# Optimization experiments

Measured on AMD Instinct MI355X. Metric: run time of the kernel, lower is better.

The kernel has to match this reference:

```python
import jax, jax.numpy as jnp
import numpy as np

N, F_IN, HID, H1, NG = 50000, 128, 64, 4, 512
E = 800000


def setup_inputs() -> dict:
    key = jax.random.key(0)
    ks = jax.random.split(key, 16)
    x = jax.random.normal(ks[0], (N, F_IN), dtype=jnp.float32)
    edge_index = jax.random.randint(ks[1], (2, E), 0, N, dtype=jnp.int64)
    batch = jnp.sort(jax.random.randint(ks[2], (N,), 0, NG, dtype=jnp.int64))
    s = 0.05
    W1 = jax.random.normal(ks[3], (F_IN, H1 * HID), dtype=jnp.float32) * s
    a_src1 = jax.random.normal(ks[4], (H1, HID), dtype=jnp.float32) * s
    a_dst1 = jax.random.normal(ks[5], (H1, HID), dtype=jnp.float32) * s
    b1 = jnp.zeros((H1 * HID,), dtype=jnp.float32)
    W2 = jax.random.normal(ks[6], (H1 * HID, HID), dtype=jnp.float32) * s
    a_src2 = jax.random.normal(ks[7], (1, HID), dtype=jnp.float32) * s
    a_dst2 = jax.random.normal(ks[8], (1, HID), dtype=jnp.float32) * s
    b2 = jnp.zeros((HID,), dtype=jnp.float32)
    Wc = jax.random.normal(ks[9], (HID, 2), dtype=jnp.float32) * s
    bc = jnp.zeros((2,), dtype=jnp.float32)
    return dict(x=x, edge_index=edge_index, batch=batch, W1=W1, a_src1=a_src1,
                a_dst1=a_dst1, b1=b1, W2=W2, a_src2=a_src2, a_dst2=a_dst2,
                b2=b2, Wc=Wc, bc=bc)


def gat_layer(x, W, a_src, a_dst, bias, src, dst, n):
    # PyG GATConv: h = x @ W per head; e_ij = LeakyReLU(a_src.h_j + a_dst.h_i),
    # softmax over incoming edges of each dst node, then scatter-add aggregate.
    H, D = a_src.shape
    h = (x @ W).reshape(n, H, D)                       # [N,H,D]
    asrc = jnp.einsum('nhd,hd->nh', h, a_src)          # [N,H]
    adst = jnp.einsum('nhd,hd->nh', h, a_dst)
    e = jax.nn.leaky_relu(asrc[src] + adst[dst], 0.2)  # [E,H]
    m = jax.lax.stop_gradient(jax.ops.segment_max(e, dst, num_segments=n))
    p = jnp.exp(e - m[dst])
    s = jax.ops.segment_sum(p, dst, num_segments=n)
    alpha = p / (s[dst] + 1e-16)                       # [E,H]
    out = jax.ops.segment_sum(alpha[:, :, None] * h[src], dst, num_segments=n)
    return out.reshape(n, H * D) + bias


def reference(x, edge_index, batch, W1, a_src1, a_dst1, b1, W2, a_src2, a_dst2, b2, Wc, bc):
    n = x.shape[0]
    loops = jnp.arange(n, dtype=edge_index.dtype)
    src = jnp.concatenate([edge_index[0], loops])  # add self-loops (PyG default)
    dst = jnp.concatenate([edge_index[1], loops])
    h = jax.nn.relu(gat_layer(x, W1, a_src1, a_dst1, b1, src, dst, n))
    h = jax.nn.relu(gat_layer(h, W2, a_src2, a_dst2, b2, src, dst, n))
    # global mean pool over graphs
    ng = NG
    sums = jax.ops.segment_sum(h, batch, num_segments=ng)
    cnts = jax.ops.segment_sum(jnp.ones((n,), h.dtype), batch, num_segments=ng)
    pooled = sums / jnp.maximum(cnts, 1.0)[:, None]
    logits = pooled @ Wc + bc
    return jax.nn.log_softmax(logits, axis=1)
```

## Files before the change

kernel.cpp:

```cpp
#include <hip/hip_runtime.h>
#include <hip/hip_bf16.h>
#include <cstddef>
#include <cstdint>

#define FIN   128
#define HID   64
#define H1    4
#define NGRAPH 512
#define BCAP  8192

typedef short bf16x8 __attribute__((ext_vector_type(8)));
typedef float f32x4  __attribute__((ext_vector_type(4)));

#if defined(__has_builtin)
#if __has_builtin(__builtin_amdgcn_cvt_f32_fp8) && __has_builtin(__builtin_amdgcn_cvt_pk_fp8_f32)
#define HAVE_HW_FP8 1
#endif
#endif

__device__ __forceinline__ float wave_reduce_sum(float v) {
  #pragma unroll
  for (int off = 32; off > 0; off >>= 1) v += __shfl_down(v, off, 64);
  return v;
}

__device__ __forceinline__ float leaky02(float x) {
  return x > 0.0f ? x : 0.2f * x;
}

__device__ __forceinline__ unsigned short f2bf(float f) {
  union { float f; unsigned int i; } v; v.f = f;
  unsigned int b = v.i;
  return (unsigned short)((b + 0x7FFFu + ((b >> 16) & 1u)) >> 16);
}

#ifndef HAVE_HW_FP8
__device__ __forceinline__ unsigned char f2fp8_1(float f) {
  unsigned int u = __float_as_uint(f);
  unsigned int s = u >> 31;
  u &= 0x7fffffffu;
  if (u > 0x43e00000u) u = 0x43e00000u;
  unsigned int b = u + (0x0007FFFFu + ((u >> 20) & 1u));
  int e = (int)(b >> 23) - 127;
  unsigned int m = (b >> 20) & 7u;
  unsigned char o;
  if (e < -9) o = 0;
  else if (e < -6) { int sh = -6 - e; o = (unsigned char)((8u | m) >> sh); }
  else if (e > 8) o = 0x7e;
  else o = (unsigned char)(((e + 7) << 3) | m);
  return o | (unsigned char)(s << 7);
}
__device__ __forceinline__ float fp8tof_1(unsigned char b) {
  unsigned int s = b >> 7, e = (b >> 3) & 15u, m = b & 7u;
  float v = (e == 0) ? (float)m * 0.001953125f
                     : (float)(8u + m) * __uint_as_float((117u + e) << 23);
  return s ? -v : v;
}
#endif

__device__ __forceinline__ unsigned char f2fp8(float f) {
#ifdef HAVE_HW_FP8
  return (unsigned char)(__builtin_amdgcn_cvt_pk_fp8_f32(f, f, 0u, false) & 0xffu);
#else
  return f2fp8_1(f);
#endif
}
__device__ __forceinline__ float fp8dec(unsigned int w, int i) {
#ifdef HAVE_HW_FP8
  switch (i) {
    case 0: return __builtin_amdgcn_cvt_f32_fp8(w, 0);
    case 1: return __builtin_amdgcn_cvt_f32_fp8(w, 1);
    case 2: return __builtin_amdgcn_cvt_f32_fp8(w, 2);
    default: return __builtin_amdgcn_cvt_f32_fp8(w, 3);
  }
#else
  return fp8tof_1((unsigned char)((w >> (8 * i)) & 0xffu));
#endif
}

#define P3K 16
__global__ __launch_bounds__(256)
void bpart_kernel(const int* __restrict__ src, const int* __restrict__ dst,
                  int* __restrict__ bucketFill, unsigned int* __restrict__ bucketBuf,
                  const float* __restrict__ W1, const float* __restrict__ W2,
                  unsigned short* __restrict__ W1T, unsigned short* __restrict__ W2T,
                  const int* __restrict__ batch, int* __restrict__ gstart,
                  int* __restrict__ gend, int E, int N, int nbuck) {
  int tid = threadIdx.x;
  int stride = gridDim.x * 256;
  int t0 = blockIdx.x * 256 + tid;
  for (int u = t0; u < 256 * 128; u += stride) {
    int n = u >> 7, k = u & 127;
    W1T[u] = f2bf(W1[(size_t)k * 256 + n]);
  }
  for (int u = t0; u < 64 * 256; u += stride) {
    int n = u >> 8, k = u & 255;
    W2T[u] = f2bf(W2[(size_t)k * 64 + n]);
  }
  for (int i = t0; i < N; i += stride) {
    int g = batch[i];
    if (i == 0 || batch[i - 1] != g) gstart[g] = i;
    if (i == N - 1 || batch[i + 1] != g) gend[g] = i + 1;
  }

  __shared__ int lhist[256];
  __shared__ int lbase[256];
  int chunk = 256 * P3K;
  for (int start = blockIdx.x * chunk; start < E; start += gridDim.x * chunk) {
    lhist[tid] = 0;
    __syncthreads();
    int mybuck[P3K]; unsigned int mypack[P3K]; int myrank[P3K];
    #pragma unroll
    for (int k = 0; k < P3K; k++) {
      int i = start + k * 256 + tid;
      if (i < E) {
        int d = dst[i];
        int b = d >> 8;
        mybuck[k] = b;
        mypack[k] = (unsigned int)src[i] | ((unsigned int)(d & 255) << 16);
        myrank[k] = atomicAdd(&lhist[b], 1);
      } else mybuck[k] = -1;
    }
    __syncthreads();
    if (tid < nbuck) lbase[tid] = (lhist[tid] > 0) ? atomicAdd(&bucketFill[tid], lhist[tid]) : 0;
    __syncthreads();
    #pragma unroll
    for (int k = 0; k < P3K; k++) {
      if (mybuck[k] >= 0) {
        int b = mybuck[k];
        int pos = lbase[b] + myrank[k];
        if (pos < BCAP) bucketBuf[((size_t)b << 13) + pos] = mypack[k];
      }
    }
    __syncthreads();
  }
}

__global__ __launch_bounds__(256)
void bbuild_kernel(const unsigned int* __restrict__ bucketBuf, const int* __restrict__ bucketFill,
                   int* __restrict__ rowstart, int* __restrict__ rowend,
                   unsigned short* __restrict__ csr, int N) {
  __shared__ int ldeg[256];
  __shared__ int lscan[256];
  __shared__ int lfill[256];
  int b = blockIdx.x;
  int tid = threadIdx.x;
  int r0 = b << 13;
  int cnt = bucketFill[b]; if (cnt > BCAP) cnt = BCAP;
  int nb0 = b << 8;
  ldeg[tid] = 0;
  __syncthreads();
  for (int j = tid; j < cnt; j += 256)
    atomicAdd(&ldeg[bucketBuf[r0 + j] >> 16], 1);
  __syncthreads();
  int v = ldeg[tid];
  lscan[tid] = v;
  __syncthreads();
  for (int off = 1; off < 256; off <<= 1) {
    int u = (tid >= off) ? lscan[tid - off] : 0;
    __syncthreads();
    lscan[tid] += u;
    __syncthreads();
  }
  int excl = lscan[tid] - v;
  lfill[tid] = excl;
  if (nb0 + tid < N) {
    rowstart[nb0 + tid] = r0 + excl;
    rowend[nb0 + tid]   = r0 + excl + v;
  }
  __syncthreads();
  for (int j = tid; j < cnt; j += 256) {
    unsigned int p = bucketBuf[r0 + j];
    int pos = r0 + atomicAdd(&lfill[p >> 16], 1);
    csr[pos] = (unsigned short)(p & 0xffffu);
  }
}

__global__ __launch_bounds__(256)
void gemm1_kernel(const float* __restrict__ X, const unsigned short* __restrict__ W1T,
                  unsigned char* __restrict__ h1f8,
                  const float* __restrict__ a_src, const float* __restrict__ a_dst,
                  float* __restrict__ asv, float* __restrict__ adv, int N) {
  __shared__ unsigned short As[64][136];
  __shared__ unsigned short Bs[256][40];
  int t = threadIdx.x;
  int w = t >> 6, lane = t & 63;
  int quad = lane >> 4, l16 = lane & 15;
  int blockRow = blockIdx.x * 64;

  {
    int node = t >> 2, kp = (t & 3) * 32;
    int gn = blockRow + node; if (gn >= N) gn = N - 1;
    const float4* xp = (const float4*)(X + (size_t)gn * 128 + kp);
    #pragma unroll
    for (int i = 0; i < 4; i++) {
      float4 va = xp[2 * i], vb = xp[2 * i + 1];
      union { unsigned short u[8]; uint4 v; } r;
      r.u[0] = f2bf(va.x); r.u[1] = f2bf(va.y); r.u[2] = f2bf(va.z); r.u[3] = f2bf(va.w);
      r.u[4] = f2bf(vb.x); r.u[5] = f2bf(vb.y); r.u[6] = f2bf(vb.z); r.u[7] = f2bf(vb.w);
      *(uint4*)&As[node][kp + i * 8] = r.v;
    }
  }

  f32x4 acc[4][4];
  #pragma unroll
  for (int i = 0; i < 4; i++)
    #pragma unroll
    for (int j = 0; j < 4; j++) acc[i][j] = (f32x4){0.f, 0.f, 0.f, 0.f};

  for (int kc = 0; kc < FIN; kc += 32) {
    {
      const unsigned short* wp = W1T + (size_t)t * 128 + kc;
      #pragma unroll
      for (int i = 0; i < 4; i++) {
        uint4 v = *(const uint4*)(wp + i * 8);
        *(uint4*)&Bs[t][i * 8] = v;
      }
    }
    __syncthreads();
    bf16x8 af[4], bfr[4];
    #pragma unroll
    for (int mt = 0; mt < 4; mt++)
      af[mt] = *(const bf16x8*)&As[mt * 16 + l16][kc + quad * 8];
    #pragma unroll
    for (int nt = 0; nt < 4; nt++)
      bfr[nt] = *(const bf16x8*)&Bs[w * 64 + nt * 16 + l16][quad * 8];
    #pragma unroll
    for (int mt = 0; mt < 4; mt++)
      #pragma unroll
      for (int nt = 0; nt < 4; nt++)
        acc[mt][nt] = __builtin_amdgcn_mfma_f32_16x16x32_bf16(af[mt], bfr[nt], acc[mt][nt], 0, 0, 0);
    __syncthreads();
  }

  float a_s[4], a_d[4];
  #pragma unroll
  for (int nt = 0; nt < 4; nt++) {
    a_s[nt] = a_src[w * 64 + nt * 16 + l16];
    a_d[nt] = a_dst[w * 64 + nt * 16 + l16];
  }
  #pragma unroll
  for (int mt = 0; mt < 4; mt++) {
    #pragma unroll
    for (int reg = 0; reg < 4; reg++) {
      int node = blockRow + mt * 16 + quad * 4 + reg;
      bool ok = node < N;
      float ps = 0.0f, pd = 0.0f;
      #pragma unroll
      for (int nt = 0; nt < 4; nt++) {
        float v = acc[mt][nt][reg];
        ps = fmaf(v, a_s[nt], ps);
        pd = fmaf(v, a_d[nt], pd);
        if (ok) h1f8[(size_t)node * 256 + w * 64 + nt * 16 + l16] = f2fp8(v);
      }
      #pragma unroll
      for (int off = 8; off > 0; off >>= 1) {
        ps += __shfl_xor(ps, off, 16);
        pd += __shfl_xor(pd, off, 16);
      }
      if (l16 == 0 && ok) {
        asv[(size_t)node * 4 + w] = ps;
        adv[(size_t)node * 4 + w] = pd;
      }
    }
  }
}

__global__ __launch_bounds__(256)
void gemm2_kernel(const unsigned short* __restrict__ out1b, const unsigned short* __restrict__ W2T,
                  unsigned char* __restrict__ h2f8,
                  const float* __restrict__ a_src, const float* __restrict__ a_dst,
                  float* __restrict__ asv, float* __restrict__ adv, int N) {
  __shared__ unsigned short As[64][40];
  __shared__ unsigned short Bs[64][40];
  int t = threadIdx.x;
  int w = t >> 6, lane = t & 63;
  int quad = lane >> 4, l16 = lane & 15;
  int blockRow = blockIdx.x * 64;

  f32x4 acc[4];
  #pragma unroll
  for (int j = 0; j < 4; j++) acc[j] = (f32x4){0.f, 0.f, 0.f, 0.f};

  int nodeS = t >> 2, koff = (t & 3) * 8;
  int gnS = blockRow + nodeS; if (gnS >= N) gnS = N - 1;

  for (int kc = 0; kc < 256; kc += 32) {
    {
      uint4 va = *(const uint4*)(out1b + (size_t)gnS * 256 + kc + koff);
      *(uint4*)&As[nodeS][koff] = va;
      uint4 vb = *(const uint4*)(W2T + (size_t)nodeS * 256 + kc + koff);
      *(uint4*)&Bs[nodeS][koff] = vb;
    }
    __syncthreads();
    bf16x8 af = *(const bf16x8*)&As[w * 16 + l16][quad * 8];
    #pragma unroll
    for (int nt = 0; nt < 4; nt++) {
      bf16x8 bfr = *(const bf16x8*)&Bs[nt * 16 + l16][quad * 8];
      acc[nt] = __builtin_amdgcn_mfma_f32_16x16x32_bf16(af, bfr, acc[nt], 0, 0, 0);
    }
    __syncthreads();
  }

  float a_s[4], a_d[4];
  #pragma unroll
  for (int nt = 0; nt < 4; nt++) {
    a_s[nt] = a_src[nt * 16 + l16];
    a_d[nt] = a_dst[nt * 16 + l16];
  }
  #pragma unroll
  for (int reg = 0; reg < 4; reg++) {
    int node = blockRow + w * 16 + quad * 4 + reg;
    bool ok = node < N;
    float ps = 0.0f, pd = 0.0f;
    #pragma unroll
    for (int nt = 0; nt < 4; nt++) {
      float v = acc[nt][reg];
      ps = fmaf(v, a_s[nt], ps);
      pd = fmaf(v, a_d[nt], pd);
      if (ok) h2f8[(size_t)node * 64 + nt * 16 + l16] = f2fp8(v);
    }
    #pragma unroll
    for (int off = 8; off > 0; off >>= 1) {
      ps += __shfl_xor(ps, off, 16);
      pd += __shfl_xor(pd, off, 16);
    }
    if (l16 == 0 && ok) { asv[node] = ps; adv[node] = pd; }
  }
}

__global__ __launch_bounds__(256)
void agg1_kernel(const unsigned char* __restrict__ h1f8, const int* __restrict__ rowstart,
                 const int* __restrict__ rowend, const unsigned short* __restrict__ csr,
                 const float* __restrict__ asv, const float* __restrict__ adv,
                 const float* __restrict__ b1, unsigned short* __restrict__ out1b, int N) {
  __shared__ int   sbuf[4][64];
  __shared__ float pbuf[4][4][68];
  int wv   = threadIdx.x >> 6;
  int lane = threadIdx.x & 63;
  int n = blockIdx.x * 4 + wv;
  if (n >= N) return;
  int r0 = rowstart[n], r1 = rowend[n];
  float4 ad = *(const float4*)(adv + (size_t)n * 4);
  float4 asn = *(const float4*)(asv + (size_t)n * 4);
  int hsel = lane >> 4;

  float es0 = leaky02(asn.x + ad.x);
  float es1 = leaky02(asn.y + ad.y);
  float es2 = leaky02(asn.z + ad.z);
  float es3 = leaky02(asn.w + ad.w);
  float esel = hsel == 0 ? es0 : (hsel == 1 ? es1 : (hsel == 2 ? es2 : es3));

  float q0 = 0, q1 = 0, q2 = 0, q3 = 0;
  float a0 = 0, a1 = 0, a2 = 0, a3 = 0;

  for (int base = r0; base < r1; base += 64) {
    int j = base + lane;
    int cnt = min(64, r1 - base);
    if (j < r1) {
      int s = csr[j];
      float4 as = *(const float4*)(asv + (size_t)s * 4);
      sbuf[wv][lane] = s;
      float p0 = __expf(leaky02(as.x + ad.x));
      float p1 = __expf(leaky02(as.y + ad.y));
      float p2 = __expf(leaky02(as.z + ad.z));
      float p3 = __expf(leaky02(as.w + ad.w));
      pbuf[wv][0][lane] = p0;
      pbuf[wv][1][lane] = p1;
      pbuf[wv][2][lane] = p2;
      pbuf[wv][3][lane] = p3;
      q0 += p0; q1 += p1; q2 += p2; q3 += p3;
    }
    __threadfence_block();

    int c = 0;
    for (; c + 4 <= cnt; c += 4) {
      int4 sv = *(const int4*)&sbuf[wv][c];
      int sc0 = __builtin_amdgcn_readfirstlane(sv.x);
      int sc1 = __builtin_amdgcn_readfirstlane(sv.y);
      int sc2 = __builtin_amdgcn_readfirstlane(sv.z);
      int sc3 = __builtin_amdgcn_readfirstlane(sv.w);
      unsigned int hw0 = *((const unsigned int*)(h1f8 + ((size_t)sc0 << 8)) + lane);
      unsigned int hw1 = *((const unsigned int*)(h1f8 + ((size_t)sc1 << 8)) + lane);
      unsigned int hw2 = *((const unsigned int*)(h1f8 + ((size_t)sc2 << 8)) + lane);
      unsigned int hw3 = *((const unsigned int*)(h1f8 + ((size_t)sc3 << 8)) + lane);
      float4 pv = *(const float4*)&pbuf[wv][hsel][c];
      a0 = fmaf(pv.x, fp8dec(hw0, 0), a0);
      a1 = fmaf(pv.x, fp8dec(hw0, 1), a1);
      a2 = fmaf(pv.x, fp8dec(hw0, 2), a2);
      a3 = fmaf(pv.x, fp8dec(hw0, 3), a3);
      a0 = fmaf(pv.y, fp8dec(hw1, 0), a0);
      a1 = fmaf(pv.y, fp8dec(hw1, 1), a1);
      a2 = fmaf(pv.y, fp8dec(hw1, 2), a2);
      a3 = fmaf(pv.y, fp8dec(hw1, 3), a3);
      a0 = fmaf(pv.z, fp8dec(hw2, 0), a0);
      a1 = fmaf(pv.z, fp8dec(hw2, 1), a1);
      a2 = fmaf(pv.z, fp8dec(hw2, 2), a2);
      a3 = fmaf(pv.z, fp8dec(hw2, 3), a3);
      a0 = fmaf(pv.w, fp8dec(hw3, 0), a0);
      a1 = fmaf(pv.w, fp8dec(hw3, 1), a1);
      a2 = fmaf(pv.w, fp8dec(hw3, 2), a2);
      a3 = fmaf(pv.w, fp8dec(hw3, 3), a3);
    }
    for (; c < cnt; c++) {
      int sc = __builtin_amdgcn_readfirstlane(sbuf[wv][c]);
      float psel = pbuf[wv][hsel][c];
      unsigned int hw = *((const unsigned int*)(h1f8 + ((size_t)sc << 8)) + lane);
      a0 = fmaf(psel, fp8dec(hw, 0), a0);
      a1 = fmaf(psel, fp8dec(hw, 1), a1);
      a2 = fmaf(psel, fp8dec(hw, 2), a2);
      a3 = fmaf(psel, fp8dec(hw, 3), a3);
    }
    __threadfence_block();
  }

  #pragma unroll
  for (int off = 32; off > 0; off >>= 1) {
    q0 += __shfl_xor(q0, off, 64);
    q1 += __shfl_xor(q1, off, 64);
    q2 += __shfl_xor(q2, off, 64);
    q3 += __shfl_xor(q3, off, 64);
  }
  float ssum = hsel == 0 ? q0 : (hsel == 1 ? q1 : (hsel == 2 ? q2 : q3));

  {
    float psel = __expf(esel);
    ssum += psel;
    unsigned int hw = *((const unsigned int*)(h1f8 + ((size_t)n << 8)) + lane);
    a0 = fmaf(psel, fp8dec(hw, 0), a0);
    a1 = fmaf(psel, fp8dec(hw, 1), a1);
    a2 = fmaf(psel, fp8dec(hw, 2), a2);
    a3 = fmaf(psel, fp8dec(hw, 3), a3);
  }

  float inv = 1.0f / (ssum + 1e-16f);
  int d0 = lane * 4;
  float4 bv = *(const float4*)(b1 + d0);
  float v0 = a0 * inv + bv.x;
  float v1 = a1 * inv + bv.y;
  float v2 = a2 * inv + bv.z;
  float v3 = a3 * inv + bv.w;
  ushort4 o;
  o.x = f2bf(v0 > 0 ? v0 : 0.0f);
  o.y = f2bf(v1 > 0 ? v1 : 0.0f);
  o.z = f2bf(v2 > 0 ? v2 : 0.0f);
  o.w = f2bf(v3 > 0 ? v3 : 0.0f);
  *(ushort4*)(out1b + (size_t)n * 256 + d0) = o;
}

__global__ __launch_bounds__(256)
void agg2_kernel(const unsigned char* __restrict__ h2f8, const int* __restrict__ rowstart,
                 const int* __restrict__ rowend, const unsigned short* __restrict__ csr,
                 const float* __restrict__ asv, const float* __restrict__ adv,
                 const float* __restrict__ b2, float* __restrict__ h2out, int N) {
  __shared__ int   sbuf[4][64];
  __shared__ float pbuf[4][64];
  int wv   = threadIdx.x >> 6;
  int lane = threadIdx.x & 63;
  int quad = lane >> 4, l16 = lane & 15;
  int n = blockIdx.x * 4 + wv;
  if (n >= N) return;
  int r0 = rowstart[n], r1 = rowend[n];
  float ad = adv[n];
  float eself = leaky02(asv[n] + ad);
  float q = 0.0f;
  float a0 = 0, a1 = 0, a2 = 0, a3 = 0;

  for (int base = r0; base < r1; base += 64) {
    int j = base + lane;
    int cnt = min(64, r1 - base);
    if (j < r1) {
      int s = csr[j];
      sbuf[wv][lane] = s;
      float p = __expf(leaky02(asv[s] + ad));
      pbuf[wv][lane] = p;
      q += p;
    }
    __threadfence_block();

    int c = 0;
    for (; c + 8 <= cnt; c += 8) {
      int scA = sbuf[wv][c + quad];
      int scB = sbuf[wv][c + 4 + quad];
      float pA = pbuf[wv][c + quad];
      float pB = pbuf[wv][c + 4 + quad];
      unsigned int hwA = *((const unsigned int*)(h2f8 + ((size_t)scA << 6)) + l16);
      unsigned int hwB = *((const unsigned int*)(h2f8 + ((size_t)scB << 6)) + l16);
      a0 = fmaf(pA, fp8dec(hwA, 0), a0);
      a1 = fmaf(pA, fp8dec(hwA, 1), a1);
      a2 = fmaf(pA, fp8dec(hwA, 2), a2);
      a3 = fmaf(pA, fp8dec(hwA, 3), a3);
      a0 = fmaf(pB, fp8dec(hwB, 0), a0);
      a1 = fmaf(pB, fp8dec(hwB, 1), a1);
      a2 = fmaf(pB, fp8dec(hwB, 2), a2);
      a3 = fmaf(pB, fp8dec(hwB, 3), a3);
    }
    for (; c + 4 <= cnt; c += 4) {
      int sc = sbuf[wv][c + quad];
      float p1 = pbuf[wv][c + quad];
      unsigned int hw = *((const unsigned int*)(h2f8 + ((size_t)sc << 6)) + l16);
      a0 = fmaf(p1, fp8dec(hw, 0), a0);
      a1 = fmaf(p1, fp8dec(hw, 1), a1);
      a2 = fmaf(p1, fp8dec(hw, 2), a2);
      a3 = fmaf(p1, fp8dec(hw, 3), a3);
    }
    int rem = cnt - c;
    if (quad < rem) {
      int sc = sbuf[wv][c + quad];
      float p1 = pbuf[wv][c + quad];
      unsigned int hw = *((const unsigned int*)(h2f8 + ((size_t)sc << 6)) + l16);
      a0 = fmaf(p1, fp8dec(hw, 0), a0);
      a1 = fmaf(p1, fp8dec(hw, 1), a1);
      a2 = fmaf(p1, fp8dec(hw, 2), a2);
      a3 = fmaf(p1, fp8dec(hw, 3), a3);
    }
    __threadfence_block();
  }

  #pragma unroll
  for (int off = 32; off > 0; off >>= 1) q += __shfl_xor(q, off, 64);
  #pragma unroll
  for (int off = 16; off <= 32; off <<= 1) {
    a0 += __shfl_xor(a0, off, 64);
    a1 += __shfl_xor(a1, off, 64);
    a2 += __shfl_xor(a2, off, 64);
    a3 += __shfl_xor(a3, off, 64);
  }
  float ssum = q;

  {
    float p = __expf(eself);
    ssum += p;
    unsigned int hw = *((const unsigned int*)(h2f8 + ((size_t)n << 6)) + l16);
    a0 = fmaf(p, fp8dec(hw, 0), a0);
    a1 = fmaf(p, fp8dec(hw, 1), a1);
    a2 = fmaf(p, fp8dec(hw, 2), a2);
    a3 = fmaf(p, fp8dec(hw, 3), a3);
  }

  if (quad == 0) {
    float inv = 1.0f / (ssum + 1e-16f);
    float4 bv = *(const float4*)(b2 + l16 * 4);
    float4 o;
    float v0 = a0 * inv + bv.x;
    float v1 = a1 * inv + bv.y;
    float v2 = a2 * inv + bv.z;
    float v3 = a3 * inv + bv.w;
    o.x = v0 > 0 ? v0 : 0.0f;
    o.y = v1 > 0 ? v1 : 0.0f;
    o.z = v2 > 0 ? v2 : 0.0f;
    o.w = v3 > 0 ? v3 : 0.0f;
    *(float4*)(h2out + (size_t)n * 64 + l16 * 4) = o;
  }
}

__global__ __launch_bounds__(256)
void pool_kernel(const float* __restrict__ h2, const int* __restrict__ gstart,
                 const int* __restrict__ gend, const float* __restrict__ Wc,
                 const float* __restrict__ bc, float* __restrict__ out) {
  int g = blockIdx.x;
  int w = threadIdx.x >> 6, lane = threadIdx.x & 63;
  int s = gstart[g], e = gend[g];
  float acc = 0.0f;
  for (int n = s + w; n < e; n += 4) acc += h2[(size_t)n * 64 + lane];
  __shared__ float red[4][64];
  red[w][lane] = acc;
  __syncthreads();
  if (w == 0) {
    float v = red[0][lane] + red[1][lane] + red[2][lane] + red[3][lane];
    float pooled = (e > s) ? v / (float)(e - s) : 0.0f;
    float l0 = wave_reduce_sum(pooled * Wc[lane * 2 + 0]);
    float l1 = wave_reduce_sum(pooled * Wc[lane * 2 + 1]);
    if (lane == 0) {
      l0 += bc[0]; l1 += bc[1];
      float mx = fmaxf(l0, l1);
      float lse = mx + logf(__expf(l0 - mx) + __expf(l1 - mx));
      out[g * 2 + 0] = l0 - lse;
      out[g * 2 + 1] = l1 - lse;
    }
  }
}

extern "C" void kernel_launch(void* const* d_in, const int* in_sizes, int n_in,
                              void* d_out, int out_size, void* d_ws, size_t ws_size,
                              hipStream_t stream) {
  const float* x      = (const float*)d_in[0];
  const int*   ei     = (const int*)d_in[1];
  const int*   batch  = (const int*)d_in[2];
  const float* W1     = (const float*)d_in[3];
  const float* a_src1 = (const float*)d_in[4];
  const float* a_dst1 = (const float*)d_in[5];
  const float* b1     = (const float*)d_in[6];
  const float* W2     = (const float*)d_in[7];
  const float* a_src2 = (const float*)d_in[8];
  const float* a_dst2 = (const float*)d_in[9];
  const float* b2     = (const float*)d_in[10];
  const float* Wc     = (const float*)d_in[11];
  const float* bc     = (const float*)d_in[12];
  float* out = (float*)d_out;

  const int N = in_sizes[0] / FIN;
  const int E = in_sizes[1] / 2;
  const int* srcArr = ei;
  const int* dstArr = ei + E;
  const int nbuck = (N + 255) >> 8;

  char* base = (char*)d_ws;
  size_t off = 0;
  auto alloc = [&](size_t bytes) -> void* {
    void* p = base + off;
    off = (off + bytes + 255) & ~(size_t)255;
    return p;
  };
  unsigned short* W1T  = (unsigned short*)alloc((size_t)256 * 128 * 2);
  unsigned short* W2T  = (unsigned short*)alloc((size_t)64 * 256 * 2);
  unsigned char*  h1f8 = (unsigned char*)alloc((size_t)N * 256);
  unsigned short* out1b= (unsigned short*)alloc((size_t)N * 256 * 2);
  unsigned char*  h2f8 = (unsigned char*)alloc((size_t)N * 64);
  float* h2    = (float*)alloc((size_t)N * 64 * 4);
  float* asv1  = (float*)alloc((size_t)N * 4 * 4);
  float* adv1  = (float*)alloc((size_t)N * 4 * 4);
  float* asv2  = (float*)alloc((size_t)N * 4);
  float* adv2  = (float*)alloc((size_t)N * 4);
  int*   bucketFill= (int*)alloc(256 * 4);
  int*   gstart= (int*)alloc(NGRAPH * 4);
  int*   gend  = (int*)alloc(NGRAPH * 4);
  size_t zspan = (size_t)((char*)gend + NGRAPH * 4 - (char*)bucketFill);
  int*   rowstart = (int*)alloc((size_t)N * 4);
  int*   rowend   = (int*)alloc((size_t)N * 4);
  unsigned int* bucketBuf = (unsigned int*)alloc((size_t)nbuck * BCAP * 4);
  unsigned short* csr = (unsigned short*)alloc((size_t)nbuck * BCAP * 2);
  (void)ws_size; (void)n_in; (void)out_size;

  int gridWv = (N + 3) / 4;
  int gridG  = (N + 63) / 64;
  int gridP3 = (E + 256 * P3K - 1) / (256 * P3K);

  hipMemsetAsync(bucketFill, 0, zspan, stream);
  bpart_kernel<<<gridP3, 256, 0, stream>>>(srcArr, dstArr, bucketFill, bucketBuf,
                                           W1, W2, W1T, W2T, batch, gstart, gend,
                                           E, N, nbuck);
  bbuild_kernel<<<nbuck, 256, 0, stream>>>(bucketBuf, bucketFill, rowstart, rowend, csr, N);

  gemm1_kernel<<<gridG, 256, 0, stream>>>(x, W1T, h1f8, a_src1, a_dst1, asv1, adv1, N);
  agg1_kernel<<<gridWv, 256, 0, stream>>>(h1f8, rowstart, rowend, csr, asv1, adv1, b1, out1b, N);

  gemm2_kernel<<<gridG, 256, 0, stream>>>(out1b, W2T, h2f8, a_src2, a_dst2, asv2, adv2, N);
  agg2_kernel<<<gridWv, 256, 0, stream>>>(h2f8, rowstart, rowend, csr, asv2, adv2, b2, h2, N);

  pool_kernel<<<NGRAPH, 256, 0, stream>>>(h2, gstart, gend, Wc, bc, out);
}
```

Measured before the change: 227.4 us.

## Merge CSR bucket build with first GEMM and use packed FP8 decode

Merges the CSR bucket-build kernel and the first-layer GEMM into one launch. The first nbuck blocks build CSR rows and the remaining blocks run the GEMM, with shared memory overlaid through a union. This lets the two independent stages run concurrently and removes one launch boundary. Separately, FP8 neighbor decoding in both aggregation kernels now uses the packed two-value convert builtin when it is available, halving convert instructions per 4-byte word. The union sizes shared memory to the larger GEMM layout, so the bucket-build blocks carry the GEMM's shared-memory footprint.

```diff
diff --git a/kernel.cpp b/kernel.cpp
--- a/kernel.cpp
+++ b/kernel.cpp
@@ -11,10 +11,14 @@
 
 typedef short bf16x8 __attribute__((ext_vector_type(8)));
 typedef float f32x4  __attribute__((ext_vector_type(4)));
+typedef float f32x2  __attribute__((ext_vector_type(2)));
 
 #if defined(__has_builtin)
 #if __has_builtin(__builtin_amdgcn_cvt_f32_fp8) && __has_builtin(__builtin_amdgcn_cvt_pk_fp8_f32)
 #define HAVE_HW_FP8 1
+#endif
+#if __has_builtin(__builtin_amdgcn_cvt_pk_f32_fp8)
+#define HAVE_HW_FP8_PK 1
 #endif
 #endif
 
@@ -50,13 +54,13 @@
   else o = (unsigned char)(((e + 7) << 3) | m);
   return o | (unsigned char)(s << 7);
 }
+#endif
 __device__ __forceinline__ float fp8tof_1(unsigned char b) {
   unsigned int s = b >> 7, e = (b >> 3) & 15u, m = b & 7u;
   float v = (e == 0) ? (float)m * 0.001953125f
                      : (float)(8u + m) * __uint_as_float((117u + e) << 23);
   return s ? -v : v;
 }
-#endif
 
 __device__ __forceinline__ unsigned char f2fp8(float f) {
 #ifdef HAVE_HW_FP8
@@ -65,16 +69,26 @@
   return f2fp8_1(f);
 #endif
 }
-__device__ __forceinline__ float fp8dec(unsigned int w, int i) {
-#ifdef HAVE_HW_FP8
-  switch (i) {
-    case 0: return __builtin_amdgcn_cvt_f32_fp8(w, 0);
-    case 1: return __builtin_amdgcn_cvt_f32_fp8(w, 1);
-    case 2: return __builtin_amdgcn_cvt_f32_fp8(w, 2);
-    default: return __builtin_amdgcn_cvt_f32_fp8(w, 3);
-  }
+
+__device__ __forceinline__ void fma4_fp8(unsigned int hw, float p,
+                                         float& a0, float& a1, float& a2, float& a3) {
+#ifdef HAVE_HW_FP8_PK
+  f32x2 lo = __builtin_amdgcn_cvt_pk_f32_fp8((int)hw, false);
+  f32x2 hi = __builtin_amdgcn_cvt_pk_f32_fp8((int)hw, true);
+  a0 = fmaf(p, lo.x, a0);
+  a1 = fmaf(p, lo.y, a1);
+  a2 = fmaf(p, hi.x, a2);
+  a3 = fmaf(p, hi.y, a3);
+#elif defined(HAVE_HW_FP8)
+  a0 = fmaf(p, __builtin_amdgcn_cvt_f32_fp8(hw, 0), a0);
+  a1 = fmaf(p, __builtin_amdgcn_cvt_f32_fp8(hw, 1), a1);
+  a2 = fmaf(p, __builtin_amdgcn_cvt_f32_fp8(hw, 2), a2);
+  a3 = fmaf(p, __builtin_amdgcn_cvt_f32_fp8(hw, 3), a3);
 #else
-  return fp8tof_1((unsigned char)((w >> (8 * i)) & 0xffu));
+  a0 = fmaf(p, fp8tof_1((unsigned char)(hw & 0xffu)), a0);
+  a1 = fmaf(p, fp8tof_1((unsigned char)((hw >> 8) & 0xffu)), a1);
+  a2 = fmaf(p, fp8tof_1((unsigned char)((hw >> 16) & 0xffu)), a2);
+  a3 = fmaf(p, fp8tof_1((unsigned char)((hw >> 24) & 0xffu)), a3);
 #endif
 }
 
@@ -137,56 +151,59 @@
 }
 
 __global__ __launch_bounds__(256)
-void bbuild_kernel(const unsigned int* __restrict__ bucketBuf, const int* __restrict__ bucketFill,
-                   int* __restrict__ rowstart, int* __restrict__ rowend,
-                   unsigned short* __restrict__ csr, int N) {
-  __shared__ int ldeg[256];
-  __shared__ int lscan[256];
-  __shared__ int lfill[256];
-  int b = blockIdx.x;
+void bbuild_gemm1_kernel(const unsigned int* __restrict__ bucketBuf,
+                         const int* __restrict__ bucketFill,
+                         int* __restrict__ rowstart, int* __restrict__ rowend,
+                         unsigned short* __restrict__ csr,
+                         const float* __restrict__ X, const unsigned short* __restrict__ W1T,
+                         unsigned char* __restrict__ h1f8,
+                         const float* __restrict__ a_src, const float* __restrict__ a_dst,
+                         float* __restrict__ asv, float* __restrict__ adv,
+                         int N, int nbuck) {
+  __shared__ union {
+    struct { unsigned short As[64][136]; unsigned short Bs[256][40]; } g;
+    struct { int ldeg[256]; int lscan[256]; int lfill[256]; } b;
+  } sm;
   int tid = threadIdx.x;
-  int r0 = b << 13;
-  int cnt = bucketFill[b]; if (cnt > BCAP) cnt = BCAP;
-  int nb0 = b << 8;
-  ldeg[tid] = 0;
-  __syncthreads();
-  for (int j = tid; j < cnt; j += 256)
-    atomicAdd(&ldeg[bucketBuf[r0 + j] >> 16], 1);
-  __syncthreads();
-  int v = ldeg[tid];
-  lscan[tid] = v;
-  __syncthreads();
-  for (int off = 1; off < 256; off <<= 1) {
-    int u = (tid >= off) ? lscan[tid - off] : 0;
-    __syncthreads();
-    lscan[tid] += u;
-    __syncthreads();
-  }
-  int excl = lscan[tid] - v;
-  lfill[tid] = excl;
-  if (nb0 + tid < N) {
-    rowstart[nb0 + tid] = r0 + excl;
-    rowend[nb0 + tid]   = r0 + excl + v;
-  }
-  __syncthreads();
-  for (int j = tid; j < cnt; j += 256) {
-    unsigned int p = bucketBuf[r0 + j];
-    int pos = r0 + atomicAdd(&lfill[p >> 16], 1);
-    csr[pos] = (unsigned short)(p & 0xffffu);
-  }
-}
-
-__global__ __launch_bounds__(256)
-void gemm1_kernel(const float* __restrict__ X, const unsigned short* __restrict__ W1T,
-                  unsigned char* __restrict__ h1f8,
-                  const float* __restrict__ a_src, const float* __restrict__ a_dst,
-                  float* __restrict__ asv, float* __restrict__ adv, int N) {
-  __shared__ unsigned short As[64][136];
-  __shared__ unsigned short Bs[256][40];
-  int t = threadIdx.x;
+
+  if (blockIdx.x < (unsigned)nbuck) {
+    int b = blockIdx.x;
+    int r0 = b << 13;
+    int cnt = bucketFill[b]; if (cnt > BCAP) cnt = BCAP;
+    int nb0 = b << 8;
+    sm.b.ldeg[tid] = 0;
+    __syncthreads();
+    for (int j = tid; j < cnt; j += 256)
+      atomicAdd(&sm.b.ldeg[bucketBuf[r0 + j] >> 16], 1);
+    __syncthreads();
+    int v = sm.b.ldeg[tid];
+    sm.b.lscan[tid] = v;
+    __syncthreads();
+    for (int off = 1; off < 256; off <<= 1) {
+      int u = (tid >= off) ? sm.b.lscan[tid - off] : 0;
+      __syncthreads();
+      sm.b.lscan[tid] += u;
+      __syncthreads();
+    }
+    int excl = sm.b.lscan[tid] - v;
+    sm.b.lfill[tid] = excl;
+    if (nb0 + tid < N) {
+      rowstart[nb0 + tid] = r0 + excl;
+      rowend[nb0 + tid]   = r0 + excl + v;
+    }
+    __syncthreads();
+    for (int j = tid; j < cnt; j += 256) {
+      unsigned int p = bucketBuf[r0 + j];
+      int pos = r0 + atomicAdd(&sm.b.lfill[p >> 16], 1);
+      csr[pos] = (unsigned short)(p & 0xffffu);
+    }
+    return;
+  }
+
+  int t = tid;
   int w = t >> 6, lane = t & 63;
   int quad = lane >> 4, l16 = lane & 15;
-  int blockRow = blockIdx.x * 64;
+  int blockRow = (blockIdx.x - nbuck) * 64;
 
   {
     int node = t >> 2, kp = (t & 3) * 32;
@@ -198,7 +215,7 @@
       union { unsigned short u[8]; uint4 v; } r;
       r.u[0] = f2bf(va.x); r.u[1] = f2bf(va.y); r.u[2] = f2bf(va.z); r.u[3] = f2bf(va.w);
       r.u[4] = f2bf(vb.x); r.u[5] = f2bf(vb.y); r.u[6] = f2bf(vb.z); r.u[7] = f2bf(vb.w);
-      *(uint4*)&As[node][kp + i * 8] = r.v;
+      *(uint4*)&sm.g.As[node][kp + i * 8] = r.v;
     }
   }
 
@@ -214,17 +231,17 @@
       #pragma unroll
       for (int i = 0; i < 4; i++) {
         uint4 v = *(const uint4*)(wp + i * 8);
-        *(uint4*)&Bs[t][i * 8] = v;
+        *(uint4*)&sm.g.Bs[t][i * 8] = v;
       }
     }
     __syncthreads();
     bf16x8 af[4], bfr[4];
     #pragma unroll
     for (int mt = 0; mt < 4; mt++)
-      af[mt] = *(const bf16x8*)&As[mt * 16 + l16][kc + quad * 8];
+      af[mt] = *(const bf16x8*)&sm.g.As[mt * 16 + l16][kc + quad * 8];
     #pragma unroll
     for (int nt = 0; nt < 4; nt++)
-      bfr[nt] = *(const bf16x8*)&Bs[w * 64 + nt * 16 + l16][quad * 8];
+      bfr[nt] = *(const bf16x8*)&sm.g.Bs[w * 64 + nt * 16 + l16][quad * 8];
     #pragma unroll
     for (int mt = 0; mt < 4; mt++)
       #pragma unroll
@@ -385,31 +402,16 @@
       unsigned int hw2 = *((const unsigned int*)(h1f8 + ((size_t)sc2 << 8)) + lane);
       unsigned int hw3 = *((const unsigned int*)(h1f8 + ((size_t)sc3 << 8)) + lane);
       float4 pv = *(const float4*)&pbuf[wv][hsel][c];
-      a0 = fmaf(pv.x, fp8dec(hw0, 0), a0);
-      a1 = fmaf(pv.x, fp8dec(hw0, 1), a1);
-      a2 = fmaf(pv.x, fp8dec(hw0, 2), a2);
-      a3 = fmaf(pv.x, fp8dec(hw0, 3), a3);
-      a0 = fmaf(pv.y, fp8dec(hw1, 0), a0);
-      a1 = fmaf(pv.y, fp8dec(hw1, 1), a1);
-      a2 = fmaf(pv.y, fp8dec(hw1, 2), a2);
-      a3 = fmaf(pv.y, fp8dec(hw1, 3), a3);
-      a0 = fmaf(pv.z, fp8dec(hw2, 0), a0);
-      a1 = fmaf(pv.z, fp8dec(hw2, 1), a1);
-      a2 = fmaf(pv.z, fp8dec(hw2, 2), a2);
-      a3 = fmaf(pv.z, fp8dec(hw2, 3), a3);
-      a0 = fmaf(pv.w, fp8dec(hw3, 0), a0);
-      a1 = fmaf(pv.w, fp8dec(hw3, 1), a1);
-      a2 = fmaf(pv.w, fp8dec(hw3, 2), a2);
-      a3 = fmaf(pv.w, fp8dec(hw3, 3), a3);
+      fma4_fp8(hw0, pv.x, a0, a1, a2, a3);
+      fma4_fp8(hw1, pv.y, a0, a1, a2, a3);
+      fma4_fp8(hw2, pv.z, a0, a1, a2, a3);
+      fma4_fp8(hw3, pv.w, a0, a1, a2, a3);
     }
     for (; c < cnt; c++) {
       int sc = __builtin_amdgcn_readfirstlane(sbuf[wv][c]);
       float psel = pbuf[wv][hsel][c];
       unsigned int hw = *((const unsigned int*)(h1f8 + ((size_t)sc << 8)) + lane);
-      a0 = fmaf(psel, fp8dec(hw, 0), a0);
-      a1 = fmaf(psel, fp8dec(hw, 1), a1);
-      a2 = fmaf(psel, fp8dec(hw, 2), a2);
-      a3 = fmaf(psel, fp8dec(hw, 3), a3);
+      fma4_fp8(hw, psel, a0, a1, a2, a3);
     }
     __threadfence_block();
   }
@@ -427,10 +429,7 @@
     float psel = __expf(esel);
     ssum += psel;
     unsigned int hw = *((const unsigned int*)(h1f8 + ((size_t)n << 8)) + lane);
-    a0 = fmaf(psel, fp8dec(hw, 0), a0);
-    a1 = fmaf(psel, fp8dec(hw, 1), a1);
-    a2 = fmaf(psel, fp8dec(hw, 2), a2);
-    a3 = fmaf(psel, fp8dec(hw, 3), a3);
+    fma4_fp8(hw, psel, a0, a1, a2, a3);
   }
 
   float inv = 1.0f / (ssum + 1e-16f);
@@ -486,33 +485,21 @@
       float pB = pbuf[wv][c + 4 + quad];
       unsigned int hwA = *((const unsigned int*)(h2f8 + ((size_t)scA << 6)) + l16);
       unsigned int hwB = *((const unsigned int*)(h2f8 + ((size_t)scB << 6)) + l16);
-      a0 = fmaf(pA, fp8dec(hwA, 0), a0);
-      a1 = fmaf(pA, fp8dec(hwA, 1), a1);
-      a2 = fmaf(pA, fp8dec(hwA, 2), a2);
-      a3 = fmaf(pA, fp8dec(hwA, 3), a3);
-      a0 = fmaf(pB, fp8dec(hwB, 0), a0);
-      a1 = fmaf(pB, fp8dec(hwB, 1), a1);
-      a2 = fmaf(pB, fp8dec(hwB, 2), a2);
-      a3 = fmaf(pB, fp8dec(hwB, 3), a3);
+      fma4_fp8(hwA, pA, a0, a1, a2, a3);
+      fma4_fp8(hwB, pB, a0, a1, a2, a3);
     }
     for (; c + 4 <= cnt; c += 4) {
       int sc = sbuf[wv][c + quad];
       float p1 = pbuf[wv][c + quad];
       unsigned int hw = *((const unsigned int*)(h2f8 + ((size_t)sc << 6)) + l16);
-      a0 = fmaf(p1, fp8dec(hw, 0), a0);
-      a1 = fmaf(p1, fp8dec(hw, 1), a1);
-      a2 = fmaf(p1, fp8dec(hw, 2), a2);
-      a3 = fmaf(p1, fp8dec(hw, 3), a3);
+      fma4_fp8(hw, p1, a0, a1, a2, a3);
     }
     int rem = cnt - c;
     if (quad < rem) {
       int sc = sbuf[wv][c + quad];
       float p1 = pbuf[wv][c + quad];
       unsigned int hw = *((const unsigned int*)(h2f8 + ((size_t)sc << 6)) + l16);
-      a0 = fmaf(p1, fp8dec(hw, 0), a0);
-      a1 = fmaf(p1, fp8dec(hw, 1), a1);
-      a2 = fmaf(p1, fp8dec(hw, 2), a2);
-      a3 = fmaf(p1, fp8dec(hw, 3), a3);
+      fma4_fp8(hw, p1, a0, a1, a2, a3);
     }
     __threadfence_block();
   }
@@ -532,10 +519,7 @@
     float p = __expf(eself);
     ssum += p;
     unsigned int hw = *((const unsigned int*)(h2f8 + ((size_t)n << 6)) + l16);
-    a0 = fmaf(p, fp8dec(hw, 0), a0);
-    a1 = fmaf(p, fp8dec(hw, 1), a1);
-    a2 = fmaf(p, fp8dec(hw, 2), a2);
-    a3 = fmaf(p, fp8dec(hw, 3), a3);
+    fma4_fp8(hw, p, a0, a1, a2, a3);
   }
 
   if (quad == 0) {
@@ -640,9 +624,9 @@
   bpart_kernel<<<gridP3, 256, 0, stream>>>(srcArr, dstArr, bucketFill, bucketBuf,
                                            W1, W2, W1T, W2T, batch, gstart, gend,
                                            E, N, nbuck);
-  bbuild_kernel<<<nbuck, 256, 0, stream>>>(bucketBuf, bucketFill, rowstart, rowend, csr, N);
-
-  gemm1_kernel<<<gridG, 256, 0, stream>>>(x, W1T, h1f8, a_src1, a_dst1, asv1, adv1, N);
+  bbuild_gemm1_kernel<<<nbuck + gridG, 256, 0, stream>>>(
+      bucketBuf, bucketFill, rowstart, rowend, csr,
+      x, W1T, h1f8, a_src1, a_dst1, asv1, adv1, N, nbuck);
   agg1_kernel<<<gridWv, 256, 0, stream>>>(h1f8, rowstart, rowend, csr, asv1, adv1, b1, out1b, N);
 
   gemm2_kernel<<<gridG, 256, 0, stream>>>(out1b, W2T, h2f8, a_src2, a_dst2, asv2, adv2, N);
```

Result: faster. 218.8 us (-3.8%).
